# Kernel optimization log

Measured on AMD Instinct MI355X. Metric: run time of the kernel, lower is better.

The kernel has to match this reference:

```python
import jax, jax.numpy as jnp
import numpy as np

D_MODEL = 1024
NHEAD = 16
D_HEAD = D_MODEL // NHEAD


def setup_inputs() -> dict:
    key = jax.random.key(0)
    ks = jax.random.split(key, 5)
    s_in = 1.0 / np.sqrt(D_MODEL)
    x = jax.random.normal(ks[0], (2, 2048, D_MODEL), dtype=jnp.float32)
    Wqkv = jax.random.uniform(ks[1], (D_MODEL, 3 * D_MODEL), jnp.float32, -s_in, s_in)
    bqkv = jax.random.uniform(ks[2], (3 * D_MODEL,), jnp.float32, -s_in, s_in)
    Wproj = jax.random.uniform(ks[3], (D_MODEL, D_MODEL), jnp.float32, -s_in, s_in)
    bproj = jax.random.uniform(ks[4], (D_MODEL,), jnp.float32, -s_in, s_in)
    return {"x": x, "Wqkv": Wqkv, "bqkv": bqkv, "Wproj": Wproj, "bproj": bproj}


def reference(x, Wqkv, bqkv, Wproj, bproj):
    B, N, D = x.shape
    qkv = x @ Wqkv + bqkv                       # [B, N, 3D]
    q, k, v = jnp.split(qkv, 3, axis=-1)
    # [B, N, D] -> [B, H, N, d]
    def to_heads(t):
        return t.reshape(B, N, NHEAD, D_HEAD).transpose(0, 2, 1, 3)
    q, k, v = to_heads(q), to_heads(k), to_heads(v)
    scale = 1.0 / np.sqrt(D_HEAD).astype(np.float32)
    attn = jnp.einsum('bhqd,bhkd->bhqk', q, k) * scale
    attn = jax.nn.softmax(attn, axis=-1)
    y = jnp.einsum('bhqk,bhkd->bhqd', attn, v)  # [B, H, N, d]
    y = y.transpose(0, 2, 1, 3).reshape(B, N, D)
    return y @ Wproj + bproj
```

## Files before the change

### kernel.cpp

```cpp
#include <hip/hip_runtime.h>
#include <hip/hip_bf16.h>
#include <stdint.h>

typedef __hip_bfloat16 bf16;
typedef __attribute__((ext_vector_type(8))) short short8;
typedef __attribute__((ext_vector_type(4))) float f32x4;

#define QSCALE 0.18033688011f

__device__ __forceinline__ float fast_exp2(float x) {
#if __has_builtin(__builtin_amdgcn_exp2f)
  return __builtin_amdgcn_exp2f(x);
#else
  return exp2f(x);
#endif
}

__device__ __forceinline__ uint32_t pack2_bf16(float a, float b) {
#if __has_builtin(__builtin_amdgcn_cvt_pk_bf16_f32)
  typedef __attribute__((ext_vector_type(2))) __bf16 bf16x2;
  bf16x2 v = __builtin_amdgcn_cvt_pk_bf16_f32(a, b);
  return __builtin_bit_cast(uint32_t, v);
#else
  uint32_t ua = __builtin_bit_cast(uint32_t, a);
  uint32_t ub = __builtin_bit_cast(uint32_t, b);
  ua += 0x7FFF + ((ua >> 16) & 1);
  ub += 0x7FFF + ((ub >> 16) & 1);
  return (ua >> 16) | (ub & 0xFFFF0000u);
#endif
}

__device__ __forceinline__ void gload_lds16(const bf16* g, bf16* l) {
#if __has_builtin(__builtin_amdgcn_global_load_lds)
  __builtin_amdgcn_global_load_lds(
      (const __attribute__((address_space(1))) void*)(uintptr_t)g,
      (__attribute__((address_space(3))) void*)(uint32_t)(uintptr_t)l,
      16, 0, 0);
#else
  int lane = threadIdx.x & 63;
  *(short8*)(l + lane * 8) = *(const short8*)(g + lane * 8);
#endif
}

__device__ __forceinline__ void transpose_tile(const float* __restrict__ in,
                                               bf16* __restrict__ out,
                                               int R, int C, int bx, int by,
                                               bf16 (*t)[72]) {
  const int r0 = by * 64, c0 = bx * 64;
  const int rr = threadIdx.x >> 3, cc = (threadIdx.x & 7) * 8;
#pragma unroll
  for (int rep = 0; rep < 2; ++rep) {
    int y = rr + rep * 32;
    const float* p = in + (size_t)(r0 + y) * C + c0 + cc;
    f32x4 v0 = *(const f32x4*)p;
    f32x4 v1 = *(const f32x4*)(p + 4);
#pragma unroll
    for (int j = 0; j < 4; ++j) {
      t[cc + j][y] = __float2bfloat16(v0[j]);
      t[cc + 4 + j][y] = __float2bfloat16(v1[j]);
    }
  }
  __syncthreads();
#pragma unroll
  for (int rep = 0; rep < 2; ++rep) {
    int y = rr + rep * 32;
    short8 v = *(const short8*)&t[y][cc];
    *(short8*)(out + (size_t)(c0 + y) * R + r0 + cc) = v;
  }
}

__global__ __launch_bounds__(256)
void prep_k(const float* __restrict__ x, bf16* __restrict__ xb,
            const float* __restrict__ Wqkv, bf16* __restrict__ WtQkv,
            const float* __restrict__ Wproj, bf16* __restrict__ WtP) {
  __shared__ __align__(16) bf16 t[64][72];
  const int bid = blockIdx.x;
  if (bid < 2048) {
    int i = (bid * 256 + threadIdx.x) * 8;
    f32x4 v0 = *(const f32x4*)(x + i);
    f32x4 v1 = *(const f32x4*)(x + i + 4);
    short8 r;
    bf16* rb = (bf16*)&r;
#pragma unroll
    for (int j = 0; j < 4; ++j) {
      rb[j] = __float2bfloat16(v0[j]);
      rb[4 + j] = __float2bfloat16(v1[j]);
    }
    *(short8*)(xb + i) = r;
  } else if (bid < 2048 + 768) {
    int b = bid - 2048;
    transpose_tile(Wqkv, WtQkv, 1024, 3072, b % 48, b / 48, t);
  } else {
    int b = bid - 2816;
    transpose_tile(Wproj, WtP, 1024, 1024, b % 16, b / 16, t);
  }
}

template <int MODE, int TM>
__global__ __launch_bounds__(256, 2)
void gemm_bt(const bf16* __restrict__ A, const bf16* __restrict__ Bt,
             const float* __restrict__ bias, float* __restrict__ outp,
             bf16* __restrict__ Qd, bf16* __restrict__ Kd, bf16* __restrict__ Vt,
             int M, int Nn, int K) {
  constexpr int MI = TM / 32;
  __shared__ __align__(16) bf16 As[TM * 32];
  __shared__ __align__(16) bf16 Bs[128 * 32];

  const int tid = threadIdx.x;
  const int wave = tid >> 6, lane = tid & 63;
  const int quad = lane >> 4, l16 = lane & 15;
  const int mw = (wave >> 1) * (TM / 2), nw = (wave & 1) * 64;
  const int m_blk = blockIdx.y * TM, n_blk = blockIdx.x * 128;

  f32x4 acc[MI][4];
#pragma unroll
  for (int i = 0; i < MI; ++i)
#pragma unroll
    for (int j = 0; j < 4; ++j) acc[i][j] = (f32x4){0.f, 0.f, 0.f, 0.f};

  const int rowA = lane >> 2, colA = (lane & 3) * 8;
  const int chunkB = wave * 2;
  const bf16* gB = Bt + (size_t)(n_blk + chunkB * 16 + rowA) * K + colA;
  bf16* lB0 = &Bs[chunkB * 16 * 32];
  bf16* lB1 = &Bs[(chunkB + 1) * 16 * 32];

  const int chunkA = (TM == 128) ? wave * 2 : wave;
  const bf16* gA = A + (size_t)(m_blk + chunkA * 16 + rowA) * K + colA;
  bf16* lA0 = &As[chunkA * 16 * 32];
  bf16* lA1 = &As[(chunkA + 1) * 16 * 32];

  for (int kt = 0; kt < K; kt += 32) {
    gload_lds16(gA, lA0);
    if (TM == 128) gload_lds16(gA + 16 * K, lA1);
    gload_lds16(gB, lB0);
    gload_lds16(gB + 16 * K, lB1);
    gA += 32; gB += 32;
    __syncthreads();
    short8 af[MI], bfv[4];
#pragma unroll
    for (int i = 0; i < MI; ++i)
      af[i] = *(const short8*)&As[(mw + i * 16 + l16) * 32 + quad * 8];
#pragma unroll
    for (int j = 0; j < 4; ++j)
      bfv[j] = *(const short8*)&Bs[(nw + j * 16 + l16) * 32 + quad * 8];
#pragma unroll
    for (int i = 0; i < MI; ++i)
#pragma unroll
      for (int j = 0; j < 4; ++j)
        acc[i][j] = __builtin_amdgcn_mfma_f32_16x16x32_bf16(af[i], bfv[j],
                                                            acc[i][j], 0, 0, 0);
    __syncthreads();
  }

#pragma unroll
  for (int j = 0; j < 4; ++j) {
    const int ncol = n_blk + nw + j * 16 + l16;
    const float bval = bias[ncol];
    if (MODE == 0) {
      const int part = ncol >> 10;
      const int rem = ncol & 1023;
      const int h = rem >> 6, dh = rem & 63;
#pragma unroll
      for (int i = 0; i < MI; ++i) {
        const int t0 = m_blk + mw + i * 16 + quad * 4;
        const int b = t0 >> 11, tt = t0 & 2047;
        const size_t bh = (size_t)(b * 16 + h);
        if (part == 2) {
          uint32_t w0 = pack2_bf16(acc[i][j][0] + bval, acc[i][j][1] + bval);
          uint32_t w1 = pack2_bf16(acc[i][j][2] + bval, acc[i][j][3] + bval);
          uint2 pk; pk.x = w0; pk.y = w1;
          *(uint2*)&Vt[(bh * 64 + dh) * 2048 + tt] = pk;
        } else {
          bf16* dst = (part == 0) ? Qd : Kd;
          const float sc = (part == 0) ? QSCALE : 1.0f;
#pragma unroll
          for (int r = 0; r < 4; ++r)
            dst[(bh * 2048 + tt + r) * 64 + dh] =
                __float2bfloat16((acc[i][j][r] + bval) * sc);
        }
      }
    } else {
#pragma unroll
      for (int i = 0; i < MI; ++i) {
        const int mrow0 = m_blk + mw + i * 16 + quad * 4;
#pragma unroll
        for (int r = 0; r < 4; ++r)
          outp[(size_t)(mrow0 + r) * Nn + ncol] = acc[i][j][r] + bval;
      }
    }
  }
}

__global__ __launch_bounds__(256, 4)
void attn_kernel(const bf16* __restrict__ Qg, const bf16* __restrict__ Kg,
                 const bf16* __restrict__ Vt, bf16* __restrict__ yg) {
  __shared__ __align__(16) bf16 Ks[64][72];
  __shared__ __align__(16) bf16 Vts[64 * 72];
  __shared__ __align__(16) bf16 Ps[64][72];

  const int tid = threadIdx.x;
  const int wave = tid >> 6, lane = tid & 63;
  const int quad = lane >> 4, l16 = lane & 15;
  const int m0 = wave * 16;

  const int bx = blockIdx.x;
  const int qt = bx & 31;
  const int bh = bx >> 5;

  const bf16* Qb = Qg + ((size_t)bh * 2048 + qt * 64) * 64;
  const bf16* Kb = Kg + (size_t)bh * 2048 * 64;
  const bf16* Vtb = Vt + (size_t)bh * 64 * 2048;

  short8 qf[2];
#pragma unroll
  for (int kb = 0; kb < 2; ++kb)
    qf[kb] = *(const short8*)(Qb + (size_t)(m0 + l16) * 64 + kb * 32 + quad * 8);

  f32x4 yacc[4];
#pragma unroll
  for (int nb = 0; nb < 4; ++nb) yacc[nb] = (f32x4){0.f, 0.f, 0.f, 0.f};

  float sum_l = 0.f;

  const int kr = tid >> 3, kc = (tid & 7) * 8;
  const int vdd = tid & 63, vo = tid >> 6;
  const int voff0 = vdd * 72 + (((vo) + (vdd >> 3)) & 7) * 8;
  const int voff1 = vdd * 72 + (((vo + 4) + (vdd >> 3)) & 7) * 8;

  const bf16* Kp0 = Kb + (size_t)kr * 64 + kc;
  const bf16* Kp1 = Kb + (size_t)(kr + 32) * 64 + kc;
  const bf16* Vp0 = Vtb + (size_t)vdd * 2048 + vo * 8;
  const bf16* Vp1 = Vtb + (size_t)vdd * 2048 + (vo + 4) * 8;

  short8 gk0 = *(const short8*)Kp0;
  short8 gk1 = *(const short8*)Kp1;
  short8 gv0 = *(const short8*)Vp0;
  short8 gv1 = *(const short8*)Vp1;

  for (int kt = 0; kt < 2048; kt += 64) {
    *(short8*)&Ks[kr][kc] = gk0;
    *(short8*)&Ks[kr + 32][kc] = gk1;
    *(short8*)&Vts[voff0] = gv0;
    *(short8*)&Vts[voff1] = gv1;
    __syncthreads();

    if (kt + 64 < 2048) {
      gk0 = *(const short8*)(Kp0 + (size_t)(kt + 64) * 64);
      gk1 = *(const short8*)(Kp1 + (size_t)(kt + 64) * 64);
      gv0 = *(const short8*)(Vp0 + kt + 64);
      gv1 = *(const short8*)(Vp1 + kt + 64);
    }

    f32x4 st[4];
#pragma unroll
    for (int i = 0; i < 4; ++i) {
      short8 kf0 = *(const short8*)&Ks[i * 16 + l16][quad * 8];
      short8 kf1 = *(const short8*)&Ks[i * 16 + l16][32 + quad * 8];
      f32x4 a = (f32x4){0.f, 0.f, 0.f, 0.f};
      a = __builtin_amdgcn_mfma_f32_16x16x32_bf16(kf0, qf[0], a, 0, 0, 0);
      a = __builtin_amdgcn_mfma_f32_16x16x32_bf16(kf1, qf[1], a, 0, 0, 0);
      st[i] = a;
    }

    float ssum = 0.f;
#pragma unroll
    for (int i = 0; i < 4; ++i) {
      float p0 = fast_exp2(st[i][0]);
      float p1 = fast_exp2(st[i][1]);
      float p2 = fast_exp2(st[i][2]);
      float p3 = fast_exp2(st[i][3]);
      ssum += (p0 + p1) + (p2 + p3);
      uint2 pk;
      pk.x = pack2_bf16(p0, p1);
      pk.y = pack2_bf16(p2, p3);
      *(uint2*)&Ps[m0 + l16][i * 16 + quad * 4] = pk;
    }
    sum_l += ssum;
    asm volatile("s_waitcnt lgkmcnt(0)" ::: "memory");

#pragma unroll
    for (int kb = 0; kb < 2; ++kb) {
      short8 pa = *(const short8*)&Ps[m0 + l16][kb * 32 + quad * 8];
#pragma unroll
      for (int nb = 0; nb < 4; ++nb) {
        const int d = nb * 16 + l16;
        short8 vbf = *(const short8*)&Vts[d * 72 +
            (((kb * 4 + quad) + (d >> 3)) & 7) * 8];
        yacc[nb] =
            __builtin_amdgcn_mfma_f32_16x16x32_bf16(pa, vbf, yacc[nb], 0, 0, 0);
      }
    }
    __syncthreads();
  }

  sum_l += __shfl_xor(sum_l, 16);
  sum_l += __shfl_xor(sum_l, 32);

  const int b = bh >> 4, h = bh & 15;
  const size_t rowbase = (size_t)b * 2048 + qt * 64;
#pragma unroll
  for (int r = 0; r < 4; ++r) {
    const float lv = __shfl(sum_l, quad * 4 + r, 16);
    const float inv = 1.f / lv;
    const int rr = m0 + quad * 4 + r;
#pragma unroll
    for (int nb = 0; nb < 4; ++nb)
      yg[(rowbase + rr) * 1024 + h * 64 + nb * 16 + l16] =
          __float2bfloat16(yacc[nb][r] * inv);
  }
}

extern "C" void kernel_launch(void* const* d_in, const int* in_sizes, int n_in,
                              void* d_out, int out_size, void* d_ws, size_t ws_size,
                              hipStream_t stream) {
  const float* x = (const float*)d_in[0];
  const float* Wqkv = (const float*)d_in[1];
  const float* bqkv = (const float*)d_in[2];
  const float* Wproj = (const float*)d_in[3];
  const float* bproj = (const float*)d_in[4];
  float* out = (float*)d_out;

  if (ws_size < (size_t)40 * 1024 * 1024) return;

  char* ws = (char*)d_ws;
  bf16* xb    = (bf16*)(ws + 0);
  bf16* yd    = (bf16*)(ws + 0);
  bf16* WtQkv = (bf16*)(ws + 8388608);
  bf16* WtP   = (bf16*)(ws + 14680064);
  bf16* Qd    = (bf16*)(ws + 16777216);
  bf16* Kd    = (bf16*)(ws + 25165824);
  bf16* Vten  = (bf16*)(ws + 33554432);

  prep_k<<<3072, 256, 0, stream>>>(x, xb, Wqkv, WtQkv, Wproj, WtP);
  gemm_bt<0, 128><<<dim3(24, 32), 256, 0, stream>>>(
      xb, WtQkv, bqkv, nullptr, Qd, Kd, Vten, 4096, 3072, 1024);
  attn_kernel<<<dim3(1024), 256, 0, stream>>>(Qd, Kd, Vten, yd);
  gemm_bt<1, 64><<<dim3(8, 64), 256, 0, stream>>>(
      yd, WtP, bproj, out, nullptr, nullptr, nullptr, 4096, 1024, 1024);
}
```

Baseline: 199.0 us.

## Load K fragments directly from global into registers, double-buffer V in LDS

K tiles no longer go through shared memory. Each wave loads its MFMA K fragments straight from global memory into registers and prefetches the next tile. V is double-buffered in LDS so the next tile can be stored during the current iteration, which drops the barrier at the start of each loop. The aim is less LDS traffic and fewer syncs, at the cost of every wave reading all of K from global/L2 (four times redundant) and holding more registers.

```diff
diff --git a/kernel.cpp b/kernel.cpp
--- a/kernel.cpp
+++ b/kernel.cpp
@@ -194,8 +194,7 @@
 __global__ __launch_bounds__(256, 4)
 void attn_kernel(const bf16* __restrict__ Qg, const bf16* __restrict__ Kg,
                  const bf16* __restrict__ Vt, bf16* __restrict__ yg) {
-  __shared__ __align__(16) bf16 Ks[64][72];
-  __shared__ __align__(16) bf16 Vts[64 * 72];
+  __shared__ __align__(16) bf16 Vts[2][64 * 72];
   __shared__ __align__(16) bf16 Ps[64][72];
 
   const int tid = threadIdx.x;
@@ -222,44 +221,49 @@
 
   float sum_l = 0.f;
 
-  const int kr = tid >> 3, kc = (tid & 7) * 8;
+  const bf16* Kfp = Kb + (size_t)l16 * 64 + quad * 8;
+
   const int vdd = tid & 63, vo = tid >> 6;
   const int voff0 = vdd * 72 + (((vo) + (vdd >> 3)) & 7) * 8;
   const int voff1 = vdd * 72 + (((vo + 4) + (vdd >> 3)) & 7) * 8;
-
-  const bf16* Kp0 = Kb + (size_t)kr * 64 + kc;
-  const bf16* Kp1 = Kb + (size_t)(kr + 32) * 64 + kc;
   const bf16* Vp0 = Vtb + (size_t)vdd * 2048 + vo * 8;
   const bf16* Vp1 = Vtb + (size_t)vdd * 2048 + (vo + 4) * 8;
 
-  short8 gk0 = *(const short8*)Kp0;
-  short8 gk1 = *(const short8*)Kp1;
+  short8 kf[4][2];
+#pragma unroll
+  for (int i = 0; i < 4; ++i) {
+    kf[i][0] = *(const short8*)(Kfp + (size_t)i * 16 * 64);
+    kf[i][1] = *(const short8*)(Kfp + (size_t)i * 16 * 64 + 32);
+  }
   short8 gv0 = *(const short8*)Vp0;
   short8 gv1 = *(const short8*)Vp1;
+  *(short8*)&Vts[0][voff0] = gv0;
+  *(short8*)&Vts[0][voff1] = gv1;
+  gv0 = *(const short8*)(Vp0 + 64);
+  gv1 = *(const short8*)(Vp1 + 64);
+  __syncthreads();
 
   for (int kt = 0; kt < 2048; kt += 64) {
-    *(short8*)&Ks[kr][kc] = gk0;
-    *(short8*)&Ks[kr + 32][kc] = gk1;
-    *(short8*)&Vts[voff0] = gv0;
-    *(short8*)&Vts[voff1] = gv1;
-    __syncthreads();
+    const int cur = (kt >> 6) & 1;
+    const bf16* vcur = Vts[cur];
+    bf16* vnxt = (bf16*)Vts[cur ^ 1];
+
+    f32x4 st[4];
+#pragma unroll
+    for (int i = 0; i < 4; ++i) {
+      f32x4 a = (f32x4){0.f, 0.f, 0.f, 0.f};
+      a = __builtin_amdgcn_mfma_f32_16x16x32_bf16(kf[i][0], qf[0], a, 0, 0, 0);
+      a = __builtin_amdgcn_mfma_f32_16x16x32_bf16(kf[i][1], qf[1], a, 0, 0, 0);
+      st[i] = a;
+    }
 
     if (kt + 64 < 2048) {
-      gk0 = *(const short8*)(Kp0 + (size_t)(kt + 64) * 64);
-      gk1 = *(const short8*)(Kp1 + (size_t)(kt + 64) * 64);
-      gv0 = *(const short8*)(Vp0 + kt + 64);
-      gv1 = *(const short8*)(Vp1 + kt + 64);
-    }
-
-    f32x4 st[4];
-#pragma unroll
-    for (int i = 0; i < 4; ++i) {
-      short8 kf0 = *(const short8*)&Ks[i * 16 + l16][quad * 8];
-      short8 kf1 = *(const short8*)&Ks[i * 16 + l16][32 + quad * 8];
-      f32x4 a = (f32x4){0.f, 0.f, 0.f, 0.f};
-      a = __builtin_amdgcn_mfma_f32_16x16x32_bf16(kf0, qf[0], a, 0, 0, 0);
-      a = __builtin_amdgcn_mfma_f32_16x16x32_bf16(kf1, qf[1], a, 0, 0, 0);
-      st[i] = a;
+      const bf16* kn = Kfp + (size_t)(kt + 64) * 64;
+#pragma unroll
+      for (int i = 0; i < 4; ++i) {
+        kf[i][0] = *(const short8*)(kn + (size_t)i * 16 * 64);
+        kf[i][1] = *(const short8*)(kn + (size_t)i * 16 * 64 + 32);
+      }
     }
 
     float ssum = 0.f;
@@ -276,6 +280,15 @@
       *(uint2*)&Ps[m0 + l16][i * 16 + quad * 4] = pk;
     }
     sum_l += ssum;
+
+    if (kt + 64 < 2048) {
+      *(short8*)&vnxt[voff0] = gv0;
+      *(short8*)&vnxt[voff1] = gv1;
+      if (kt + 128 < 2048) {
+        gv0 = *(const short8*)(Vp0 + kt + 128);
+        gv1 = *(const short8*)(Vp1 + kt + 128);
+      }
+    }
     asm volatile("s_waitcnt lgkmcnt(0)" ::: "memory");
 
 #pragma unroll
@@ -284,7 +297,7 @@
 #pragma unroll
       for (int nb = 0; nb < 4; ++nb) {
         const int d = nb * 16 + l16;
-        short8 vbf = *(const short8*)&Vts[d * 72 +
+        short8 vbf = *(const short8*)&vcur[d * 72 +
             (((kb * 4 + quad) + (d >> 3)) & 7) * 8];
         yacc[nb] =
             __builtin_amdgcn_mfma_f32_16x16x32_bf16(pa, vbf, yacc[nb], 0, 0, 0);
```

Measured after the change: 286.4 us. 44.0% more time.
